# Kernel tuning notes

Hardware: AMD Instinct MI355X
Metric: run time of the kernel (lower is better)

Reference implementation:

```python
import jax, jax.numpy as jnp
import numpy as np

B, N_PROP, MAX_GT = 16, 2000, 100
H = W = 160
TRAIN_ROIS = 200
ROI_POS_RATIO = 0.33
NUM_POS = int(TRAIN_ROIS * ROI_POS_RATIO)  # 66 positive slots
NUM_NEG = TRAIN_ROIS - NUM_POS
MH = MW = 28
POS_IOU_THRESH = 0.5


def _make_boxes(key, shape):
    k1, k2 = jax.random.split(key)
    y1x1 = jax.random.uniform(k1, shape + (2,), minval=0.0, maxval=0.7)
    hw = jax.random.uniform(k2, shape + (2,), minval=0.05, maxval=0.3)
    return jnp.concatenate([y1x1, y1x1 + hw], axis=-1)  # (y1,x1,y2,x2)


def _iou(boxes1, boxes2):
    # boxes1 [N,4], boxes2 [G,4] -> [N,G]
    yA = jnp.maximum(boxes1[:, None, 0], boxes2[None, :, 0])
    xA = jnp.maximum(boxes1[:, None, 1], boxes2[None, :, 1])
    yB = jnp.minimum(boxes1[:, None, 2], boxes2[None, :, 2])
    xB = jnp.minimum(boxes1[:, None, 3], boxes2[None, :, 3])
    inter = jnp.clip(yB - yA, 0.0) * jnp.clip(xB - xA, 0.0)
    a1 = (boxes1[:, 2] - boxes1[:, 0]) * (boxes1[:, 3] - boxes1[:, 1])
    a2 = (boxes2[:, 2] - boxes2[:, 0]) * (boxes2[:, 3] - boxes2[:, 1])
    union = a1[:, None] + a2[None, :] - inter
    return inter / jnp.maximum(union, 1e-10)


def _encode_deltas(rois, gt):
    h = rois[:, 2] - rois[:, 0]
    w = rois[:, 3] - rois[:, 1]
    cy = rois[:, 0] + 0.5 * h
    cx = rois[:, 1] + 0.5 * w
    gh = gt[:, 2] - gt[:, 0]
    gw = gt[:, 3] - gt[:, 1]
    gcy = gt[:, 0] + 0.5 * gh
    gcx = gt[:, 1] + 0.5 * gw
    return jnp.stack([(gcy - cy) / h, (gcx - cx) / w,
                      jnp.log(gh / h), jnp.log(gw / w)], axis=1)


def _crop_resize(img, box):
    # tf.image.crop_and_resize semantics (bilinear) for one [H,W] mask and one
    # normalized box (y1,x1,y2,x2) -> [MH,MW]
    y1, x1, y2, x2 = box
    ty = jnp.arange(MH, dtype=img.dtype) / (MH - 1)
    tx = jnp.arange(MW, dtype=img.dtype) / (MW - 1)
    ys = (y1 + ty * (y2 - y1)) * (H - 1)
    xs = (x1 + tx * (x2 - x1)) * (W - 1)
    y0f = jnp.floor(ys)
    x0f = jnp.floor(xs)
    fy = (ys - y0f)[:, None]
    fx = (xs - x0f)[None, :]
    y0 = jnp.clip(y0f.astype(jnp.int32), 0, H - 1)
    y1i = jnp.clip(y0 + 1, 0, H - 1)
    x0 = jnp.clip(x0f.astype(jnp.int32), 0, W - 1)
    x1i = jnp.clip(x0 + 1, 0, W - 1)
    return (img[y0[:, None], x0[None, :]] * (1 - fy) * (1 - fx)
            + img[y0[:, None], x1i[None, :]] * (1 - fy) * fx
            + img[y1i[:, None], x0[None, :]] * fy * (1 - fx)
            + img[y1i[:, None], x1i[None, :]] * fy * fx)


def _detection_targets_one(proposals, gt_class_ids, gt_boxes, gt_masks,
                           bbox_std_dev, key):
    # proposals [N,4], gt_class_ids [G], gt_boxes [G,4], gt_masks [H,W,G]
    valid_prop = jnp.any(proposals != 0.0, axis=1)       # trim_zeros equivalent
    valid_gt = gt_class_ids > 0
    overlaps = jnp.where(valid_gt[None, :], _iou(proposals, gt_boxes), -1.0)
    roi_iou_max = overlaps.max(axis=1)
    positive = (roi_iou_max >= POS_IOU_THRESH) & valid_prop
    negative = (roi_iou_max < POS_IOU_THRESH) & valid_prop

    # random subsampling (fixed-shape: top_k over random scores of candidates)
    kp, kn = jax.random.split(key)
    pos_scores, pos_idx = jax.lax.top_k(
        jnp.where(positive, jax.random.uniform(kp, (N_PROP,)), -1.0), NUM_POS)
    pos_valid = pos_scores > 0.0
    P = pos_valid.sum()
    # negatives keep positives at ROI_POS_RATIO of total sampled ROIs
    neg_needed = jnp.clip(
        (P.astype(jnp.float32) / ROI_POS_RATIO).astype(jnp.int32) - P, 0, NUM_NEG)
    neg_scores, neg_idx = jax.lax.top_k(
        jnp.where(negative, jax.random.uniform(kn, (N_PROP,)), -1.0), NUM_NEG)
    neg_valid = (neg_scores > 0.0) & (jnp.arange(NUM_NEG) < neg_needed)

    pos_boxes = proposals[pos_idx]                       # [NUM_POS,4]
    roi_gt_idx = jnp.argmax(overlaps[pos_idx], axis=1)   # assigned GT per ROI
    roi_gt_boxes = jnp.where(pos_valid[:, None], gt_boxes[roi_gt_idx], pos_boxes)
    roi_gt_class = jnp.where(pos_valid, gt_class_ids[roi_gt_idx], 0)

    deltas = _encode_deltas(pos_boxes, roi_gt_boxes) / bbox_std_dev[None, :]
    deltas = deltas * pos_valid[:, None]

    masks_g = jnp.transpose(gt_masks[:, :, roi_gt_idx], (2, 0, 1))  # [NUM_POS,H,W]
    crops = jax.vmap(_crop_resize)(masks_g, pos_boxes)              # [NUM_POS,MH,MW]
    masks = jnp.round(crops) * pos_valid[:, None, None]

    rois = jnp.concatenate([pos_boxes * pos_valid[:, None],
                            proposals[neg_idx] * neg_valid[:, None]], axis=0)
    class_ids = jnp.concatenate(
        [roi_gt_class, jnp.zeros((NUM_NEG,), roi_gt_class.dtype)])
    deltas = jnp.concatenate([deltas, jnp.zeros((NUM_NEG, 4), deltas.dtype)])
    masks = jnp.concatenate([masks, jnp.zeros((NUM_NEG, MH, MW), masks.dtype)])
    return rois, class_ids, deltas, masks


def detection_targets(proposals, prior_class_ids, prior_boxes, prior_masks,
                      bbox_std_dev):
    keys = jax.random.split(jax.random.key(42), B)  # per-image sampling RNG
    return jax.vmap(_detection_targets_one, in_axes=(0, 0, 0, 0, None, 0))(
        proposals, prior_class_ids, prior_boxes, prior_masks, bbox_std_dev, keys)


def setup_inputs():
    key = jax.random.key(0)
    k0, k1, k2, k3 = jax.random.split(key, 4)
    return {
        "proposals": _make_boxes(k0, (B, N_PROP)),
        "prior_class_ids": jax.random.randint(k1, (B, MAX_GT), 1, 81),
        "prior_boxes": _make_boxes(k2, (B, MAX_GT)),
        "prior_masks": (jax.random.uniform(k3, (B, H, W, MAX_GT)) > 0.5
                        ).astype(jnp.float32),
        "bbox_std_dev": jnp.array([0.1, 0.1, 0.2, 0.2], jnp.float32),
    }


def reference(proposals, prior_class_ids, prior_boxes, prior_masks,
              bbox_std_dev):
    return detection_targets(proposals, prior_class_ids, prior_boxes,
                             prior_masks, bbox_std_dev)
```

## Files before the change

kernel.cpp:

```cpp
#include <hip/hip_runtime.h>
#include <stdint.h>

#pragma clang fp contract(off)

#define NB 16
#define NPROP 2000
#define MAXGT 100
#define NUMPOS 66
#define NUMNEG 134
#define NROIS 200
#define IMH 160
#define IMW 160
#define MHH 28
#define MWW 28
#define BLK 256

#define ROIS_OFF 0
#define CLS_OFF (NB * NROIS * 4)
#define DELTA_OFF (CLS_OFF + NB * NROIS)
#define MASK_OFF (DELTA_OFF + NB * NROIS * 4)

__device__ __forceinline__ unsigned rotl32(unsigned v, int d) {
  return (v << d) | (v >> (32 - d));
}

__device__ void threefry2x32(unsigned k0, unsigned k1, unsigned c0, unsigned c1,
                             unsigned &o0, unsigned &o1) {
  const unsigned ks2 = k0 ^ k1 ^ 0x1BD11BDAu;
  unsigned x0 = c0 + k0;
  unsigned x1 = c1 + k1;
  const int rA[4] = {13, 15, 26, 6};
  const int rB[4] = {17, 29, 16, 24};
#pragma unroll
  for (int i = 0; i < 4; i++) { x0 += x1; x1 = rotl32(x1, rA[i]); x1 ^= x0; }
  x0 += k1;  x1 += ks2 + 1u;
#pragma unroll
  for (int i = 0; i < 4; i++) { x0 += x1; x1 = rotl32(x1, rB[i]); x1 ^= x0; }
  x0 += ks2; x1 += k0 + 2u;
#pragma unroll
  for (int i = 0; i < 4; i++) { x0 += x1; x1 = rotl32(x1, rA[i]); x1 ^= x0; }
  x0 += k0;  x1 += k1 + 3u;
#pragma unroll
  for (int i = 0; i < 4; i++) { x0 += x1; x1 = rotl32(x1, rB[i]); x1 ^= x0; }
  x0 += k1;  x1 += ks2 + 4u;
#pragma unroll
  for (int i = 0; i < 4; i++) { x0 += x1; x1 = rotl32(x1, rA[i]); x1 ^= x0; }
  x0 += ks2; x1 += k0 + 5u;
  o0 = x0; o1 = x1;
}

__device__ __forceinline__ float tf_uniform01(unsigned k0, unsigned k1,
                                              unsigned i) {
  unsigned a, b;
  threefry2x32(k0, k1, 0u, i, a, b);
  unsigned bits = a ^ b;
  return __uint_as_float((bits >> 9) | 0x3f800000u) - 1.0f;
}

__global__ __launch_bounds__(BLK) void dtl_score_kernel(
    const float* __restrict__ proposals,
    const int* __restrict__ gt_class,
    const float* __restrict__ gt_boxes,
    float* __restrict__ ws_pos_s,
    float* __restrict__ ws_neg_s,
    unsigned char* __restrict__ ws_arg) {
#pragma clang fp contract(off)
  const int b = blockIdx.y;
  const int i = blockIdx.x * BLK + threadIdx.x;

  __shared__ float s_gt[MAXGT][4];
  __shared__ float s_area[MAXGT];
  __shared__ int s_gtvalid[MAXGT];
  for (int g = threadIdx.x; g < MAXGT; g += BLK) {
    s_gtvalid[g] = (gt_class[b * MAXGT + g] > 0) ? 1 : 0;
    float4 gb = ((const float4*)gt_boxes)[b * MAXGT + g];
    s_gt[g][0] = gb.x; s_gt[g][1] = gb.y; s_gt[g][2] = gb.z; s_gt[g][3] = gb.w;
    s_area[g] = (gb.z - gb.x) * (gb.w - gb.y);
  }
  __syncthreads();
  if (i >= NPROP) return;

  float4 pb = ((const float4*)proposals)[b * NPROP + i];
  float p0 = pb.x, p1 = pb.y, p2 = pb.z, p3 = pb.w;
  bool vp = (p0 != 0.0f) || (p1 != 0.0f) || (p2 != 0.0f) || (p3 != 0.0f);
  float a1 = (p2 - p0) * (p3 - p1);
  float best = -2.0f;
  int arg = 0;
  for (int g = 0; g < MAXGT; ++g) {
    float yA = fmaxf(p0, s_gt[g][0]);
    float xA = fmaxf(p1, s_gt[g][1]);
    float yB = fminf(p2, s_gt[g][2]);
    float xB = fminf(p3, s_gt[g][3]);
    float inter = fmaxf(yB - yA, 0.0f) * fmaxf(xB - xA, 0.0f);
    float uni = (a1 + s_area[g]) - inter;
    float iou = inter / fmaxf(uni, 1e-10f);
    float v = s_gtvalid[g] ? iou : -1.0f;
    if (v > best) { best = v; arg = g; }
  }

  float pos_s = -1.0f, neg_s = -1.0f;
  if (vp) {
    unsigned kb0, kb1, k0, k1;
    threefry2x32(0u, 42u, 0u, (unsigned)b, kb0, kb1);
    bool pos = (best >= 0.5f);
    threefry2x32(kb0, kb1, 0u, pos ? 0u : 1u, k0, k1);
    float u = tf_uniform01(k0, k1, (unsigned)i);
    if (pos) pos_s = u; else neg_s = u;
  }
  ws_pos_s[b * NPROP + i] = pos_s;
  ws_neg_s[b * NPROP + i] = neg_s;
  ws_arg[b * NPROP + i] = (unsigned char)arg;
}

__global__ __launch_bounds__(BLK) void dtl_topk_kernel(
    const float* __restrict__ proposals,
    const int* __restrict__ gt_class,
    const float* __restrict__ gt_boxes,
    const float* __restrict__ std_dev,
    const float* __restrict__ ws_pos_s,
    const float* __restrict__ ws_neg_s,
    const unsigned char* __restrict__ ws_arg,
    float* __restrict__ out,
    int* __restrict__ ws_slots) {
#pragma clang fp contract(off)
  const int b = blockIdx.x >> 1;
  const bool is_pos = (blockIdx.x & 1) == 0;
  const int K = is_pos ? NUMPOS : NUMNEG;
  const int tid = threadIdx.x;

  __shared__ int s_hist[256];
  __shared__ int s_cand_i[NPROP];
  __shared__ float s_cand_s[NPROP];
  __shared__ int s_slot_i[NUMNEG];
  __shared__ float s_slot_s[NUMNEG];
  __shared__ float s_gt[MAXGT][4];
  __shared__ int s_gtcls[MAXGT];
  __shared__ int s_misc[4];

  const float* sc_g = (is_pos ? ws_pos_s : ws_neg_s) + (size_t)b * NPROP;
  if (is_pos) {
    for (int g = tid; g < MAXGT; g += BLK) {
      s_gtcls[g] = gt_class[b * MAXGT + g];
      float4 gb = ((const float4*)gt_boxes)[b * MAXGT + g];
      s_gt[g][0] = gb.x; s_gt[g][1] = gb.y; s_gt[g][2] = gb.z; s_gt[g][3] = gb.w;
    }
  }
  s_hist[tid] = 0;
  if (tid < 4) s_misc[tid] = 0;
  __syncthreads();

  for (int i = tid; i < NPROP; i += BLK) {
    float s = sc_g[i];
    if (s >= 0.0f) {
      int bin = (int)(s * 256.0f); if (bin > 255) bin = 255;
      atomicAdd(&s_hist[bin], 1);
    }
  }
  __syncthreads();

  if (tid < 64) {
    int l = tid;
    int h0 = s_hist[4 * l + 0], h1 = s_hist[4 * l + 1];
    int h2 = s_hist[4 * l + 2], h3 = s_hist[4 * l + 3];
    int t = h0 + h1 + h2 + h3;
    int s = t;
#pragma unroll
    for (int d = 1; d < 64; d <<= 1) {
      int v = __shfl_down(s, d, 64);
      if (l + d < 64) s += v;
    }
    int S_excl = s - t;
    int suf3 = h3 + S_excl;
    int suf2 = h2 + suf3;
    int suf1 = h1 + suf2;
    int suf0 = h0 + suf1;
    if (suf0 >= K && suf1 < K) s_misc[1] = 4 * l + 0;
    if (suf1 >= K && suf2 < K) s_misc[1] = 4 * l + 1;
    if (suf2 >= K && suf3 < K) s_misc[1] = 4 * l + 2;
    if (suf3 >= K && (l == 63 || S_excl < K)) s_misc[1] = 4 * l + 3;
  }
  for (int j = tid; j < K; j += BLK) { s_slot_i[j] = -1; s_slot_s[j] = -1.0f; }
  __syncthreads();
  const int T = s_misc[1];

  for (int i = tid; i < NPROP; i += BLK) {
    float s = sc_g[i];
    if (s >= 0.0f) {
      int bin = (int)(s * 256.0f); if (bin > 255) bin = 255;
      if (bin >= T) {
        int t = atomicAdd(&s_misc[0], 1);
        s_cand_i[t] = i; s_cand_s[t] = s;
      }
    }
  }
  __syncthreads();

  const int C = s_misc[0];
  for (int t = tid; t < C; t += BLK) {
    float st = s_cand_s[t]; int it = s_cand_i[t];
    int r = 0;
    for (int u = 0; u < C; ++u) {
      float su = s_cand_s[u];
      r += (su > st) || (su == st && s_cand_i[u] < it);
    }
    if (r < K) { s_slot_i[r] = it; s_slot_s[r] = st; }
  }
  __syncthreads();

  if (is_pos) {
    const float sd0 = std_dev[0], sd1 = std_dev[1], sd2 = std_dev[2],
                sd3 = std_dev[3];
    for (int j = tid; j < NUMPOS; j += BLK) {
      float r0 = 0, r1 = 0, r2 = 0, r3 = 0;
      float d0 = 0, d1 = 0, d2 = 0, d3 = 0;
      float cls = 0;
      int idx = s_slot_i[j];
      bool valid = (idx >= 0) && (s_slot_s[j] > 0.0f);
      int g = 0;
      if (valid) {
        float4 pb = ((const float4*)proposals)[b * NPROP + idx];
        r0 = pb.x; r1 = pb.y; r2 = pb.z; r3 = pb.w;
        g = (int)ws_arg[(size_t)b * NPROP + idx];
        float g0 = s_gt[g][0], g1 = s_gt[g][1], g2 = s_gt[g][2],
              g3 = s_gt[g][3];
        float h = r2 - r0, w = r3 - r1;
        float cy = r0 + 0.5f * h, cx = r1 + 0.5f * w;
        float gh = g2 - g0, gw = g3 - g1;
        float gcy = g0 + 0.5f * gh, gcx = g1 + 0.5f * gw;
        d0 = ((gcy - cy) / h) / sd0;
        d1 = ((gcx - cx) / w) / sd1;
        d2 = logf(gh / h) / sd2;
        d3 = logf(gw / w) / sd3;
        cls = (float)s_gtcls[g];
      }
      ws_slots[(b * NUMPOS + j) * 2 + 0] = valid ? idx : -1;
      ws_slots[(b * NUMPOS + j) * 2 + 1] = g;
      out[ROIS_OFF + (b * NROIS + j) * 4 + 0] = r0;
      out[ROIS_OFF + (b * NROIS + j) * 4 + 1] = r1;
      out[ROIS_OFF + (b * NROIS + j) * 4 + 2] = r2;
      out[ROIS_OFF + (b * NROIS + j) * 4 + 3] = r3;
      out[CLS_OFF + b * NROIS + j] = cls;
      out[DELTA_OFF + (b * NROIS + j) * 4 + 0] = d0;
      out[DELTA_OFF + (b * NROIS + j) * 4 + 1] = d1;
      out[DELTA_OFF + (b * NROIS + j) * 4 + 2] = d2;
      out[DELTA_OFF + (b * NROIS + j) * 4 + 3] = d3;
    }
  } else {
    {
      int cnt = 0;
      const float* ps = ws_pos_s + (size_t)b * NPROP;
      for (int i = tid; i < NPROP; i += BLK) cnt += (ps[i] > 0.0f) ? 1 : 0;
      atomicAdd(&s_misc[2], cnt);
    }
    __syncthreads();
    int P = s_misc[2]; P = P > NUMPOS ? NUMPOS : P;
    int t = (int)((float)P / 0.33f);
    int neg_needed = t - P;
    neg_needed = neg_needed < 0 ? 0 : neg_needed;
    neg_needed = neg_needed > NUMNEG ? NUMNEG : neg_needed;

    for (int jn = tid; jn < NUMNEG; jn += BLK) {
      int j = NUMPOS + jn;
      float r0 = 0, r1 = 0, r2 = 0, r3 = 0;
      int idx = s_slot_i[jn];
      bool valid = (idx >= 0) && (s_slot_s[jn] > 0.0f) && (jn < neg_needed);
      if (valid) {
        float4 pb = ((const float4*)proposals)[b * NPROP + idx];
        r0 = pb.x; r1 = pb.y; r2 = pb.z; r3 = pb.w;
      }
      out[ROIS_OFF + (b * NROIS + j) * 4 + 0] = r0;
      out[ROIS_OFF + (b * NROIS + j) * 4 + 1] = r1;
      out[ROIS_OFF + (b * NROIS + j) * 4 + 2] = r2;
      out[ROIS_OFF + (b * NROIS + j) * 4 + 3] = r3;
      out[CLS_OFF + b * NROIS + j] = 0.0f;
      out[DELTA_OFF + (b * NROIS + j) * 4 + 0] = 0.0f;
      out[DELTA_OFF + (b * NROIS + j) * 4 + 1] = 0.0f;
      out[DELTA_OFF + (b * NROIS + j) * 4 + 2] = 0.0f;
      out[DELTA_OFF + (b * NROIS + j) * 4 + 3] = 0.0f;
    }
  }
}

__global__ __launch_bounds__(256) void dtl_mask_kernel(
    const float* __restrict__ proposals,
    const float* __restrict__ gmasks,
    const int* __restrict__ ws_slots,
    float* __restrict__ out) {
#pragma clang fp contract(off)
  const int bs = blockIdx.x;
  const int b = bs / NROIS;
  const int slot = bs % NROIS;
  float* mo = out + MASK_OFF + (size_t)(b * NROIS + slot) * (MHH * MWW);
  int pidx = -1, g = 0;
  if (slot < NUMPOS) {
    pidx = ws_slots[(b * NUMPOS + slot) * 2 + 0];
    g = ws_slots[(b * NUMPOS + slot) * 2 + 1];
  }
  if (pidx < 0) {
    for (int p = threadIdx.x; p < MHH * MWW; p += 256) mo[p] = 0.0f;
    return;
  }
  float4 bx = ((const float4*)proposals)[b * NPROP + pidx];
  const float y1 = bx.x, x1 = bx.y, y2 = bx.z, x2 = bx.w;
  const float* img = gmasks + (size_t)b * IMH * IMW * MAXGT + g;
  for (int p = threadIdx.x; p < MHH * MWW; p += 256) {
    int m = p / MWW, n = p % MWW;
    float ty = (float)m / (float)(MHH - 1);
    float tx = (float)n / (float)(MWW - 1);
    float ys = (y1 + ty * (y2 - y1)) * (float)(IMH - 1);
    float xs = (x1 + tx * (x2 - x1)) * (float)(IMW - 1);
    float y0f = floorf(ys), x0f = floorf(xs);
    float fy = ys - y0f, fx = xs - x0f;
    int y0 = (int)y0f; y0 = y0 < 0 ? 0 : (y0 > IMH - 1 ? IMH - 1 : y0);
    int y1i = y0 + 1;  y1i = y1i > IMH - 1 ? IMH - 1 : y1i;
    int x0 = (int)x0f; x0 = x0 < 0 ? 0 : (x0 > IMW - 1 ? IMW - 1 : x0);
    int x1i = x0 + 1;  x1i = x1i > IMW - 1 ? IMW - 1 : x1i;
    float m00 = img[((size_t)y0 * IMW + x0) * MAXGT];
    float m01 = img[((size_t)y0 * IMW + x1i) * MAXGT];
    float m10 = img[((size_t)y1i * IMW + x0) * MAXGT];
    float m11 = img[((size_t)y1i * IMW + x1i) * MAXGT];
    float v = m00 * (1.0f - fy) * (1.0f - fx)
            + m01 * (1.0f - fy) * fx
            + m10 * fy * (1.0f - fx)
            + m11 * fy * fx;
    mo[p] = rintf(v);
  }
}

extern "C" void kernel_launch(void* const* d_in, const int* in_sizes, int n_in,
                              void* d_out, int out_size, void* d_ws,
                              size_t ws_size, hipStream_t stream) {
  const float* proposals = (const float*)d_in[0];
  const int* gt_class = (const int*)d_in[1];
  const float* gt_boxes = (const float*)d_in[2];
  const float* gmasks = (const float*)d_in[3];
  const float* std_dev = (const float*)d_in[4];
  float* out = (float*)d_out;

  float* ws_pos_s = (float*)d_ws;
  float* ws_neg_s = ws_pos_s + NB * NPROP;
  int* ws_slots = (int*)(ws_neg_s + NB * NPROP);
  unsigned char* ws_arg = (unsigned char*)(ws_slots + NB * NUMPOS * 2);

  dim3 g1((NPROP + BLK - 1) / BLK, NB);
  dtl_score_kernel<<<g1, BLK, 0, stream>>>(proposals, gt_class, gt_boxes,
                                           ws_pos_s, ws_neg_s, ws_arg);
  dtl_topk_kernel<<<NB * 2, BLK, 0, stream>>>(proposals, gt_class, gt_boxes,
                                              std_dev, ws_pos_s, ws_neg_s,
                                              ws_arg, out, ws_slots);
  dtl_mask_kernel<<<NB * NROIS, 256, 0, stream>>>(proposals, gmasks, ws_slots,
                                                  out);
}
```

Before: 272.1 us.

## Fuse IoU scoring into per-image top-k selection kernel

Merges the score kernel into the selection kernel. Each of the 32 blocks (pos/neg per image) now recomputes the proposal-vs-GT IoU and RNG scores into shared memory, and the block size goes to 512. This removes one launch and the global workspace round trip. In exchange, the IoU work is done by only 32 blocks instead of a wide grid, and it is duplicated across the pos and neg blocks, which reduces parallelism.

```diff
diff --git a/kernel.cpp b/kernel.cpp
--- a/kernel.cpp
+++ b/kernel.cpp
@@ -13,7 +13,7 @@
 #define IMW 160
 #define MHH 28
 #define MWW 28
-#define BLK 256
+#define SBLK 512
 
 #define ROIS_OFF 0
 #define CLS_OFF (NB * NROIS * 4)
@@ -57,69 +57,11 @@
   return __uint_as_float((bits >> 9) | 0x3f800000u) - 1.0f;
 }
 
-__global__ __launch_bounds__(BLK) void dtl_score_kernel(
-    const float* __restrict__ proposals,
-    const int* __restrict__ gt_class,
-    const float* __restrict__ gt_boxes,
-    float* __restrict__ ws_pos_s,
-    float* __restrict__ ws_neg_s,
-    unsigned char* __restrict__ ws_arg) {
-#pragma clang fp contract(off)
-  const int b = blockIdx.y;
-  const int i = blockIdx.x * BLK + threadIdx.x;
-
-  __shared__ float s_gt[MAXGT][4];
-  __shared__ float s_area[MAXGT];
-  __shared__ int s_gtvalid[MAXGT];
-  for (int g = threadIdx.x; g < MAXGT; g += BLK) {
-    s_gtvalid[g] = (gt_class[b * MAXGT + g] > 0) ? 1 : 0;
-    float4 gb = ((const float4*)gt_boxes)[b * MAXGT + g];
-    s_gt[g][0] = gb.x; s_gt[g][1] = gb.y; s_gt[g][2] = gb.z; s_gt[g][3] = gb.w;
-    s_area[g] = (gb.z - gb.x) * (gb.w - gb.y);
-  }
-  __syncthreads();
-  if (i >= NPROP) return;
-
-  float4 pb = ((const float4*)proposals)[b * NPROP + i];
-  float p0 = pb.x, p1 = pb.y, p2 = pb.z, p3 = pb.w;
-  bool vp = (p0 != 0.0f) || (p1 != 0.0f) || (p2 != 0.0f) || (p3 != 0.0f);
-  float a1 = (p2 - p0) * (p3 - p1);
-  float best = -2.0f;
-  int arg = 0;
-  for (int g = 0; g < MAXGT; ++g) {
-    float yA = fmaxf(p0, s_gt[g][0]);
-    float xA = fmaxf(p1, s_gt[g][1]);
-    float yB = fminf(p2, s_gt[g][2]);
-    float xB = fminf(p3, s_gt[g][3]);
-    float inter = fmaxf(yB - yA, 0.0f) * fmaxf(xB - xA, 0.0f);
-    float uni = (a1 + s_area[g]) - inter;
-    float iou = inter / fmaxf(uni, 1e-10f);
-    float v = s_gtvalid[g] ? iou : -1.0f;
-    if (v > best) { best = v; arg = g; }
-  }
-
-  float pos_s = -1.0f, neg_s = -1.0f;
-  if (vp) {
-    unsigned kb0, kb1, k0, k1;
-    threefry2x32(0u, 42u, 0u, (unsigned)b, kb0, kb1);
-    bool pos = (best >= 0.5f);
-    threefry2x32(kb0, kb1, 0u, pos ? 0u : 1u, k0, k1);
-    float u = tf_uniform01(k0, k1, (unsigned)i);
-    if (pos) pos_s = u; else neg_s = u;
-  }
-  ws_pos_s[b * NPROP + i] = pos_s;
-  ws_neg_s[b * NPROP + i] = neg_s;
-  ws_arg[b * NPROP + i] = (unsigned char)arg;
-}
-
-__global__ __launch_bounds__(BLK) void dtl_topk_kernel(
+__global__ __launch_bounds__(SBLK) void dtl_sel_kernel(
     const float* __restrict__ proposals,
     const int* __restrict__ gt_class,
     const float* __restrict__ gt_boxes,
     const float* __restrict__ std_dev,
-    const float* __restrict__ ws_pos_s,
-    const float* __restrict__ ws_neg_s,
-    const unsigned char* __restrict__ ws_arg,
     float* __restrict__ out,
     int* __restrict__ ws_slots) {
 #pragma clang fp contract(off)
@@ -128,34 +70,72 @@
   const int K = is_pos ? NUMPOS : NUMNEG;
   const int tid = threadIdx.x;
 
+  __shared__ float s_gt[MAXGT][4];
+  __shared__ float s_area[MAXGT];
+  __shared__ int s_gtvalid[MAXGT];
+  __shared__ int s_gtcls[MAXGT];
+  __shared__ float s_sc[NPROP];
+  __shared__ unsigned char s_arg[NPROP];
   __shared__ int s_hist[256];
   __shared__ int s_cand_i[NPROP];
   __shared__ float s_cand_s[NPROP];
   __shared__ int s_slot_i[NUMNEG];
   __shared__ float s_slot_s[NUMNEG];
-  __shared__ float s_gt[MAXGT][4];
-  __shared__ int s_gtcls[MAXGT];
   __shared__ int s_misc[4];
 
-  const float* sc_g = (is_pos ? ws_pos_s : ws_neg_s) + (size_t)b * NPROP;
-  if (is_pos) {
-    for (int g = tid; g < MAXGT; g += BLK) {
-      s_gtcls[g] = gt_class[b * MAXGT + g];
-      float4 gb = ((const float4*)gt_boxes)[b * MAXGT + g];
-      s_gt[g][0] = gb.x; s_gt[g][1] = gb.y; s_gt[g][2] = gb.z; s_gt[g][3] = gb.w;
-    }
-  }
-  s_hist[tid] = 0;
+  for (int g = tid; g < MAXGT; g += SBLK) {
+    int cls = gt_class[b * MAXGT + g];
+    s_gtcls[g] = cls;
+    s_gtvalid[g] = (cls > 0) ? 1 : 0;
+    float4 gb = ((const float4*)gt_boxes)[b * MAXGT + g];
+    s_gt[g][0] = gb.x; s_gt[g][1] = gb.y; s_gt[g][2] = gb.z; s_gt[g][3] = gb.w;
+    s_area[g] = (gb.z - gb.x) * (gb.w - gb.y);
+  }
+  if (tid < 256) s_hist[tid] = 0;
   if (tid < 4) s_misc[tid] = 0;
   __syncthreads();
 
-  for (int i = tid; i < NPROP; i += BLK) {
-    float s = sc_g[i];
-    if (s >= 0.0f) {
-      int bin = (int)(s * 256.0f); if (bin > 255) bin = 255;
+  unsigned kb0, kb1, kp0, kp1, kn0, kn1;
+  threefry2x32(0u, 42u, 0u, (unsigned)b, kb0, kb1);
+  threefry2x32(kb0, kb1, 0u, 0u, kp0, kp1);
+  threefry2x32(kb0, kb1, 0u, 1u, kn0, kn1);
+
+  int pcnt = 0;
+  for (int i = tid; i < NPROP; i += SBLK) {
+    float4 pb = ((const float4*)proposals)[b * NPROP + i];
+    float p0 = pb.x, p1 = pb.y, p2 = pb.z, p3 = pb.w;
+    bool vp = (p0 != 0.0f) || (p1 != 0.0f) || (p2 != 0.0f) || (p3 != 0.0f);
+    float a1 = (p2 - p0) * (p3 - p1);
+    float best = -2.0f;
+    int arg = 0;
+    for (int g = 0; g < MAXGT; ++g) {
+      float yA = fmaxf(p0, s_gt[g][0]);
+      float xA = fmaxf(p1, s_gt[g][1]);
+      float yB = fminf(p2, s_gt[g][2]);
+      float xB = fminf(p3, s_gt[g][3]);
+      float inter = fmaxf(yB - yA, 0.0f) * fmaxf(xB - xA, 0.0f);
+      float uni = (a1 + s_area[g]) - inter;
+      float iou = inter / fmaxf(uni, 1e-10f);
+      float v = s_gtvalid[g] ? iou : -1.0f;
+      if (v > best) { best = v; arg = g; }
+    }
+    bool pos = (best >= 0.5f) && vp;
+    bool neg = (best < 0.5f) && vp;
+    float sc = -1.0f;
+    if (is_pos) {
+      if (pos) sc = tf_uniform01(kp0, kp1, (unsigned)i);
+      s_arg[i] = (unsigned char)arg;
+    } else {
+      if (pos) pcnt += (tf_uniform01(kp0, kp1, (unsigned)i) > 0.0f) ? 1 : 0;
+      if (neg) sc = tf_uniform01(kn0, kn1, (unsigned)i);
+    }
+    s_sc[i] = sc;
+    if (sc >= 0.0f) {
+      int bin = (int)(sc * 256.0f); if (bin > 255) bin = 255;
       atomicAdd(&s_hist[bin], 1);
     }
   }
+  if (!is_pos && pcnt) atomicAdd(&s_misc[2], pcnt);
   __syncthreads();
 
   if (tid < 64) {
@@ -179,12 +159,12 @@
     if (suf2 >= K && suf3 < K) s_misc[1] = 4 * l + 2;
     if (suf3 >= K && (l == 63 || S_excl < K)) s_misc[1] = 4 * l + 3;
   }
-  for (int j = tid; j < K; j += BLK) { s_slot_i[j] = -1; s_slot_s[j] = -1.0f; }
+  for (int j = tid; j < K; j += SBLK) { s_slot_i[j] = -1; s_slot_s[j] = -1.0f; }
   __syncthreads();
   const int T = s_misc[1];
 
-  for (int i = tid; i < NPROP; i += BLK) {
-    float s = sc_g[i];
+  for (int i = tid; i < NPROP; i += SBLK) {
+    float s = s_sc[i];
     if (s >= 0.0f) {
       int bin = (int)(s * 256.0f); if (bin > 255) bin = 255;
       if (bin >= T) {
@@ -196,7 +176,7 @@
   __syncthreads();
 
   const int C = s_misc[0];
-  for (int t = tid; t < C; t += BLK) {
+  for (int t = tid; t < C; t += SBLK) {
     float st = s_cand_s[t]; int it = s_cand_i[t];
     int r = 0;
     for (int u = 0; u < C; ++u) {
@@ -210,7 +190,7 @@
   if (is_pos) {
     const float sd0 = std_dev[0], sd1 = std_dev[1], sd2 = std_dev[2],
                 sd3 = std_dev[3];
-    for (int j = tid; j < NUMPOS; j += BLK) {
+    for (int j = tid; j < NUMPOS; j += SBLK) {
       float r0 = 0, r1 = 0, r2 = 0, r3 = 0;
       float d0 = 0, d1 = 0, d2 = 0, d3 = 0;
       float cls = 0;
@@ -220,7 +200,7 @@
       if (valid) {
         float4 pb = ((const float4*)proposals)[b * NPROP + idx];
         r0 = pb.x; r1 = pb.y; r2 = pb.z; r3 = pb.w;
-        g = (int)ws_arg[(size_t)b * NPROP + idx];
+        g = (int)s_arg[idx];
         float g0 = s_gt[g][0], g1 = s_gt[g][1], g2 = s_gt[g][2],
               g3 = s_gt[g][3];
         float h = r2 - r0, w = r3 - r1;
@@ -246,20 +226,13 @@
       out[DELTA_OFF + (b * NROIS + j) * 4 + 3] = d3;
     }
   } else {
-    {
-      int cnt = 0;
-      const float* ps = ws_pos_s + (size_t)b * NPROP;
-      for (int i = tid; i < NPROP; i += BLK) cnt += (ps[i] > 0.0f) ? 1 : 0;
-      atomicAdd(&s_misc[2], cnt);
-    }
-    __syncthreads();
     int P = s_misc[2]; P = P > NUMPOS ? NUMPOS : P;
     int t = (int)((float)P / 0.33f);
     int neg_needed = t - P;
     neg_needed = neg_needed < 0 ? 0 : neg_needed;
     neg_needed = neg_needed > NUMNEG ? NUMNEG : neg_needed;
 
-    for (int jn = tid; jn < NUMNEG; jn += BLK) {
+    for (int jn = tid; jn < NUMNEG; jn += SBLK) {
       int j = NUMPOS + jn;
       float r0 = 0, r1 = 0, r2 = 0, r3 = 0;
       int idx = s_slot_i[jn];
@@ -336,18 +309,10 @@
   const float* gmasks = (const float*)d_in[3];
   const float* std_dev = (const float*)d_in[4];
   float* out = (float*)d_out;
-
-  float* ws_pos_s = (float*)d_ws;
-  float* ws_neg_s = ws_pos_s + NB * NPROP;
-  int* ws_slots = (int*)(ws_neg_s + NB * NPROP);
-  unsigned char* ws_arg = (unsigned char*)(ws_slots + NB * NUMPOS * 2);
-
-  dim3 g1((NPROP + BLK - 1) / BLK, NB);
-  dtl_score_kernel<<<g1, BLK, 0, stream>>>(proposals, gt_class, gt_boxes,
-                                           ws_pos_s, ws_neg_s, ws_arg);
-  dtl_topk_kernel<<<NB * 2, BLK, 0, stream>>>(proposals, gt_class, gt_boxes,
-                                              std_dev, ws_pos_s, ws_neg_s,
-                                              ws_arg, out, ws_slots);
+  int* ws_slots = (int*)d_ws;
+
+  dtl_sel_kernel<<<NB * 2, SBLK, 0, stream>>>(proposals, gt_class, gt_boxes,
+                                              std_dev, out, ws_slots);
   dtl_mask_kernel<<<NB * NROIS, 256, 0, stream>>>(proposals, gmasks, ws_slots,
                                                   out);
 }
```

New measurement: 305.8 us. 1.12x slower.
